# Optimization experiments

Hardware: AMD Instinct MI355X
Metric: run time of the kernel (lower is better)

The kernel has to match this reference:

```python
import jax, jax.numpy as jnp
import numpy as np

# RT-DETR multi-scale deformable attention reference (PPMSDeformableAttention forward, value_mask=None)
SPATIAL_SHAPES = ((80, 80), (40, 40), (20, 20))  # (H, W) per level; sum(H*W) = 8400 = Len_v
NUM_HEADS = 8
NUM_LEVELS = 3
NUM_POINTS = 4


def _gather_corner(v_l, ix, iy, H, W):
    # v_l: [bs, heads, H*W, hd]; ix/iy: [bs, heads, N] int32 pixel indices (possibly out of range)
    valid = (ix >= 0) & (ix < W) & (iy >= 0) & (iy < H)
    idx = jnp.clip(iy, 0, H - 1) * W + jnp.clip(ix, 0, W - 1)
    g = jnp.take_along_axis(v_l, idx[..., None], axis=2)  # [bs, heads, N, hd]
    return jnp.where(valid[..., None], g, jnp.zeros((), v_l.dtype))


def _bilinear_sample(v_l, px, py, H, W):
    # grid_sample(align_corners=False, padding_mode='zeros') semantics.
    # v_l: [bs, heads, H*W, hd]; px/py: [bs, heads, N] continuous pixel coords
    x0 = jnp.floor(px).astype(jnp.int32)
    y0 = jnp.floor(py).astype(jnp.int32)
    x1, y1 = x0 + 1, y0 + 1
    wx1 = px - x0.astype(px.dtype)
    wy1 = py - y0.astype(py.dtype)
    wx0, wy0 = 1.0 - wx1, 1.0 - wy1
    out = (_gather_corner(v_l, x0, y0, H, W) * (wx0 * wy0)[..., None]
           + _gather_corner(v_l, x1, y0, H, W) * (wx1 * wy0)[..., None]
           + _gather_corner(v_l, x0, y1, H, W) * (wx0 * wy1)[..., None]
           + _gather_corner(v_l, x1, y1, H, W) * (wx1 * wy1)[..., None])
    return out  # [bs, heads, N, hd]


def setup_inputs() -> dict:
    key = jax.random.key(0)
    ks = jax.random.split(key, 8)
    bs, Lq, C = 32, 300, 256
    Lv = sum(h * w for h, w in SPATIAL_SHAPES)
    tp = NUM_HEADS * NUM_LEVELS * NUM_POINTS  # 96
    s = 1.0 / np.sqrt(C)
    return {
        "query": jax.random.normal(ks[0], (bs, Lq, C), jnp.float32),
        "reference_points": jax.random.uniform(ks[1], (bs, Lq, NUM_LEVELS, 4), jnp.float32, 0.05, 0.95),
        "value": jax.random.normal(ks[2], (bs, Lv, C), jnp.float32),
        "Wv": jax.random.normal(ks[3], (C, C), jnp.float32) * s,
        "bv": jnp.zeros((C,), jnp.float32),
        "Woff": jax.random.normal(ks[4], (C, tp * 2), jnp.float32) * (s * 0.1),
        "boff": jax.random.normal(ks[5], (tp * 2,), jnp.float32) * 0.5,
        "Watt": jax.random.normal(ks[6], (C, tp), jnp.float32) * s,
        "batt": jnp.zeros((tp,), jnp.float32),
        "Wout": jax.random.normal(ks[7], (C, C), jnp.float32) * s,
        "bout": jnp.zeros((C,), jnp.float32),
    }


def reference(query, reference_points, value, Wv, bv, Woff, boff, Watt, batt, Wout, bout):
    bs, Lq, C = query.shape
    H_, L, P = NUM_HEADS, NUM_LEVELS, NUM_POINTS
    hd = C // H_
    Lv = value.shape[1]

    # value projection -> [bs, heads, Lv, hd]
    v = (value @ Wv + bv).reshape(bs, Lv, H_, hd).transpose(0, 2, 1, 3)

    # sampling offsets and attention weights from query
    off = (query @ Woff + boff).reshape(bs, Lq, H_, L, P, 2)
    attw = jax.nn.softmax((query @ Watt + batt).reshape(bs, Lq, H_, L * P), axis=-1)
    attw = attw.reshape(bs, Lq, H_, L, P)

    # reference_points last dim == 4: (cx, cy, w, h) normalized
    ref_xy = reference_points[:, :, None, :, None, :2]  # [bs,Lq,1,L,1,2]
    ref_wh = reference_points[:, :, None, :, None, 2:]
    loc = ref_xy + off / P * ref_wh * 0.5  # [bs,Lq,H,L,P,2], normalized [0,1]

    out = jnp.zeros((bs, Lq, H_, hd), query.dtype)
    start = 0
    for l, (H, W) in enumerate(SPATIAL_SHAPES):
        v_l = v[:, :, start:start + H * W]  # [bs, heads, H*W, hd]
        start += H * W
        # normalized -> pixel coords (align_corners=False): p = loc * size - 0.5
        locl = loc[:, :, :, l]  # [bs, Lq, heads, P, 2]
        px = locl[..., 0] * W - 0.5
        py = locl[..., 1] * H - 0.5
        # [bs, Lq, heads, P] -> [bs, heads, Lq*P]
        px = px.transpose(0, 2, 1, 3).reshape(bs, H_, Lq * P)
        py = py.transpose(0, 2, 1, 3).reshape(bs, H_, Lq * P)
        sampled = _bilinear_sample(v_l, px, py, H, W)  # [bs, heads, Lq*P, hd]
        sampled = sampled.reshape(bs, H_, Lq, P, hd)
        out = out + jnp.einsum('bhqpd,bqhp->bqhd', sampled, attw[:, :, :, l])

    out = out.reshape(bs, Lq, C)
    return out @ Wout + bout
```

## Files before the change

kernel.cpp:

```cpp
#include <hip/hip_runtime.h>
#include <hip/hip_bf16.h>

#define BS 32
#define LQ 300
#define CDIM 256
#define HEADS 8
#define HD 32
#define NLEVELS 3
#define NPOINTS 4
#define LV 8400
#define NOA 288

typedef __attribute__((ext_vector_type(4))) float f32x4;
typedef __attribute__((ext_vector_type(8))) short short8;
typedef __attribute__((ext_vector_type(8))) unsigned short u16x8;
typedef __attribute__((ext_vector_type(4))) unsigned short u16x4;

__device__ __forceinline__ unsigned short f2bf(float f) {
    __hip_bfloat16 h = __float2bfloat16(f);
    return __bfloat16_as_ushort(h);
}
__device__ __forceinline__ float bf2f(unsigned short u) {
    union { unsigned u; float f; } v; v.u = ((unsigned)u) << 16;
    return v.f;
}

__global__ void prep_weights_kernel(
    const float* __restrict__ Wv, const float* __restrict__ Wout,
    const float* __restrict__ Woff, const float* __restrict__ Watt,
    unsigned short* __restrict__ WvT, unsigned short* __restrict__ WoutT,
    unsigned short* __restrict__ WoaT)
{
    const int bid = blockIdx.x;
    const int k = threadIdx.x;
    if (bid < 256) {
        WvT[bid * 256 + k] = f2bf(Wv[k * 256 + bid]);
    } else if (bid < 512) {
        const int n = bid - 256;
        WoutT[n * 256 + k] = f2bf(Wout[k * 256 + n]);
    } else {
        const int n = bid - 512;
        const float w = (n < 192) ? Woff[k * 192 + n] : Watt[k * 96 + (n - 192)];
        WoaT[n * 256 + k] = f2bf(w);
    }
}

#define BM 128
#define BK 32
#define PAD 40
#define EP2 136
#define NT (CDIM / BK)

__global__ __launch_bounds__(256) void proj_value_mfma(
    const float* __restrict__ value, const unsigned short* __restrict__ WvT,
    const float* __restrict__ bv, unsigned short* __restrict__ vout)
{
    __shared__ alignas(16) unsigned short lds_raw[20480];
    unsigned short* lds_w = lds_raw;
    unsigned short* lds_x = lds_raw + 2 * 128 * PAD;
    unsigned short* lds_ep = lds_raw;

    const int tid = threadIdx.x;
    const int lane = tid & 63;
    const int wave = tid >> 6;
    const int wn = wave & 1;
    const int wm = wave >> 1;
    const int la = lane & 15;
    const int lg = lane >> 4;

    const int orig = blockIdx.x;
    const int xcd = orig & 7, lin = orig >> 3;
    const int bid = xcd * 525 + lin;
    const int n0 = (bid & 1) * 128;
    const long row0 = (long)(bid >> 1) * BM;

    const int sr = tid >> 1;
    const int sk = (tid & 1) * 16;
    const unsigned short* wptr = WvT + (size_t)(n0 + sr) * CDIM + sk;
    const float* xptr = value + (row0 + sr) * (long)CDIM + sk;

    u16x8 wrg[2];
    f32x4 xrg[4];

    auto load_tile = [&](int kb) {
        const u16x8* qw = (const u16x8*)(wptr + kb);
        wrg[0] = qw[0]; wrg[1] = qw[1];
        const float* p = xptr + kb;
        xrg[0] = *(const f32x4*)(p);
        xrg[1] = *(const f32x4*)(p + 4);
        xrg[2] = *(const f32x4*)(p + 8);
        xrg[3] = *(const f32x4*)(p + 12);
    };
    auto write_tile = [&](int buf) {
        u16x8* ww = (u16x8*)&lds_w[buf * (128 * PAD) + sr * PAD + sk];
        ww[0] = wrg[0]; ww[1] = wrg[1];
        u16x8 t0, t1;
#pragma unroll
        for (int i = 0; i < 4; ++i) {
            t0[i]     = f2bf(xrg[0][i]);
            t0[i + 4] = f2bf(xrg[1][i]);
            t1[i]     = f2bf(xrg[2][i]);
            t1[i + 4] = f2bf(xrg[3][i]);
        }
        u16x8* wx = (u16x8*)&lds_x[buf * (128 * PAD) + sr * PAD + sk];
        wx[0] = t0; wx[1] = t1;
    };

    f32x4 acc[4][4] = {};

    load_tile(0);
    write_tile(0);
    __syncthreads();
    int cur = 0;

    for (int t = 0; t < NT; ++t) {
        if (t + 1 < NT) load_tile((t + 1) * BK);

        const unsigned short* pw = &lds_w[cur * (128 * PAD) + (wn * 64 + la) * PAD + lg * 8];
        const unsigned short* px = &lds_x[cur * (128 * PAD) + (wm * 64 + la) * PAD + lg * 8];
        short8 xf[4];
#pragma unroll
        for (int mf = 0; mf < 4; ++mf)
            xf[mf] = *(const short8*)(px + mf * 16 * PAD);
#pragma unroll
        for (int nf = 0; nf < 4; ++nf) {
            const short8 wf = *(const short8*)(pw + nf * 16 * PAD);
#pragma unroll
            for (int mf = 0; mf < 4; ++mf)
                acc[nf][mf] = __builtin_amdgcn_mfma_f32_16x16x32_bf16(wf, xf[mf], acc[nf][mf], 0, 0, 0);
        }

        if (t + 1 < NT) write_tile(cur ^ 1);
        __syncthreads();
        cur ^= 1;
    }

#pragma unroll
    for (int nf = 0; nf < 4; ++nf) {
        const int nbl = wn * 64 + nf * 16 + lg * 4;
        const f32x4 bb = *(const f32x4*)&bv[n0 + nbl];
#pragma unroll
        for (int mf = 0; mf < 4; ++mf) {
            const int mloc = wm * 64 + mf * 16 + la;
            u16x4 o;
#pragma unroll
            for (int j = 0; j < 4; ++j) o[j] = f2bf(acc[nf][mf][j] + bb[j]);
            *(u16x4*)&lds_ep[mloc * EP2 + nbl] = o;
        }
    }
    __syncthreads();
    {
        const int er = tid >> 1;
        const int ec = (tid & 1) * 64;
        const u16x8* src = (const u16x8*)&lds_ep[er * EP2 + ec];
        u16x8* dst = (u16x8*)&vout[(row0 + er) * CDIM + n0 + ec];
#pragma unroll
        for (int i = 0; i < 8; ++i) dst[i] = src[i];
    }
}

#define APAD 40
#define BPAD 40

__global__ __launch_bounds__(256) void offatt_gemm_mfma(
    const float* __restrict__ query, const unsigned short* __restrict__ WoaT,
    const float* __restrict__ boff, const float* __restrict__ batt,
    float* __restrict__ offatt)
{
    __shared__ unsigned short lds_a[2][BM * APAD];
    __shared__ unsigned short lds_b[2][NOA * BPAD];

    const int tid = threadIdx.x;
    const int lane = tid & 63;
    const int wave = tid >> 6;
    const int wm = wave >> 1;
    const int wn = wave & 1;
    const long row0 = (long)blockIdx.x * BM;

    const int ar = tid >> 1;
    const int ak = (tid & 1) * 16;
    const float* aptr = query + (row0 + ar) * CDIM + ak;
    const unsigned short* bptr  = WoaT + (size_t)tid * CDIM;
    const unsigned short* bptr2 = WoaT + (size_t)(256 + tid) * CDIM;
    const bool extra = tid < 32;

    f32x4 arg[4];
    u16x8 brg[4], brg2[4];

    auto load_tile = [&](int kb) {
        const float* p = aptr + kb;
        arg[0] = *(const f32x4*)(p);
        arg[1] = *(const f32x4*)(p + 4);
        arg[2] = *(const f32x4*)(p + 8);
        arg[3] = *(const f32x4*)(p + 12);
        const u16x8* q = (const u16x8*)(bptr + kb);
        brg[0] = q[0]; brg[1] = q[1]; brg[2] = q[2]; brg[3] = q[3];
        if (extra) {
            const u16x8* q2 = (const u16x8*)(bptr2 + kb);
            brg2[0] = q2[0]; brg2[1] = q2[1]; brg2[2] = q2[2]; brg2[3] = q2[3];
        }
    };
    auto write_tile = [&](int buf) {
        u16x8 t0, t1;
#pragma unroll
        for (int i = 0; i < 4; ++i) {
            t0[i]     = f2bf(arg[0][i]);
            t0[i + 4] = f2bf(arg[1][i]);
            t1[i]     = f2bf(arg[2][i]);
            t1[i + 4] = f2bf(arg[3][i]);
        }
        u16x8* wa = (u16x8*)&lds_a[buf][ar * APAD + ak];
        wa[0] = t0; wa[1] = t1;
        u16x8* wb = (u16x8*)&lds_b[buf][tid * BPAD];
        wb[0] = brg[0]; wb[1] = brg[1]; wb[2] = brg[2]; wb[3] = brg[3];
        if (extra) {
            u16x8* wb2 = (u16x8*)&lds_b[buf][(256 + tid) * BPAD];
            wb2[0] = brg2[0]; wb2[1] = brg2[1]; wb2[2] = brg2[2]; wb2[3] = brg2[3];
        }
    };

    f32x4 acc[4][9] = {};
    const int la = lane & 15;
    const int lg = lane >> 4;

    load_tile(0);
    write_tile(0);
    __syncthreads();
    int cur = 0;

    for (int t = 0; t < CDIM / BK; ++t) {
        if (t + 1 < CDIM / BK) load_tile((t + 1) * BK);

        const unsigned short* pa = &lds_a[cur][(wm * 64 + la) * APAD + lg * 8];
        const unsigned short* pb = &lds_b[cur][(wn * 144 + la) * BPAD + lg * 8];
        short8 af[4];
#pragma unroll
        for (int mi = 0; mi < 4; ++mi)
            af[mi] = *(const short8*)(pa + mi * 16 * APAD);
#pragma unroll
        for (int ni = 0; ni < 9; ++ni) {
            const short8 bf = *(const short8*)(pb + ni * 16 * BPAD);
#pragma unroll
            for (int mi = 0; mi < 4; ++mi)
                acc[mi][ni] = __builtin_amdgcn_mfma_f32_16x16x32_bf16(af[mi], bf, acc[mi][ni], 0, 0, 0);
        }

        if (t + 1 < CDIM / BK) write_tile(cur ^ 1);
        __syncthreads();
        cur ^= 1;
    }

    float bias[9];
#pragma unroll
    for (int ni = 0; ni < 9; ++ni) {
        const int col = wn * 144 + ni * 16 + la;
        bias[ni] = (col < 192) ? boff[col] : batt[col - 192];
    }
#pragma unroll
    for (int mi = 0; mi < 4; ++mi) {
#pragma unroll
        for (int ni = 0; ni < 9; ++ni) {
            const int col = wn * 144 + ni * 16 + la;
#pragma unroll
            for (int j = 0; j < 4; ++j) {
                const long r = row0 + wm * 64 + mi * 16 + lg * 4 + j;
                offatt[r * NOA + col] = acc[mi][ni][j] + bias[ni];
            }
        }
    }
}

__global__ __launch_bounds__(256) void sample_kernel(
    const float* __restrict__ offatt, const float* __restrict__ refpts,
    const unsigned short* __restrict__ v, unsigned short* __restrict__ mid)
{
    __shared__ float oa_s[NOA];
    __shared__ float aw_s[96];
    __shared__ float px_s[96];
    __shared__ float py_s[96];

    const int tid = threadIdx.x;
    const int nb = blockIdx.x;
    const int x = nb & 7;
    const int rest = nb >> 3;
    const int g = rest / LQ;
    const int q = rest % LQ;
    const int b = g * 8 + x;
    const long bq = (long)b * LQ + q;

    oa_s[tid] = offatt[bq * NOA + tid];
    if (tid < 32) oa_s[256 + tid] = offatt[bq * NOA + 256 + tid];
    __syncthreads();

    if (tid < 8) {
        float m = -1e30f;
#pragma unroll
        for (int i = 0; i < 12; ++i) m = fmaxf(m, oa_s[192 + tid * 12 + i]);
        float e[12];
        float s = 0.f;
#pragma unroll
        for (int i = 0; i < 12; ++i) { e[i] = __expf(oa_s[192 + tid * 12 + i] - m); s += e[i]; }
        const float inv = 1.f / s;
#pragma unroll
        for (int i = 0; i < 12; ++i) aw_s[tid * 12 + i] = e[i] * inv;
    }
    if (tid >= 128 && tid < 224) {
        const int t = tid - 128;
        const int h = t / 12, idx = t % 12, l = idx >> 2, p = idx & 3;
        const float* rp = refpts + (bq * NLEVELS + l) * 4;
        const float rx = rp[0], ry = rp[1], rw = rp[2], rh = rp[3];
        const float ox = oa_s[((h * NLEVELS + l) * NPOINTS + p) * 2 + 0];
        const float oy = oa_s[((h * NLEVELS + l) * NPOINTS + p) * 2 + 1];
        const float lx = rx + ox * 0.125f * rw;
        const float ly = ry + oy * 0.125f * rh;
        const int Wl = 80 >> l;
        px_s[t] = lx * (float)Wl - 0.5f;
        py_s[t] = ly * (float)Wl - 0.5f;
    }
    __syncthreads();

    const int h = tid >> 5;
    const int pg = (tid >> 3) & 3;
    const int d4 = tid & 7;
    const unsigned short* vb = v + ((size_t)b * LV) * CDIM + h * HD + d4 * 4;

    float a0 = 0.f, a1 = 0.f, a2 = 0.f, a3 = 0.f;
#pragma unroll
    for (int j = 0; j < 3; ++j) {
        const int i = pg * 3 + j;
        const int l = i >> 2;
        const int idx = h * 12 + i;
        const float px = px_s[idx], py = py_s[idx], aw = aw_s[idx];
        const int Wl = 80 >> l;
        const int start = (l == 0) ? 0 : (l == 1) ? 6400 : 8000;

        const float fx = floorf(px), fy = floorf(py);
        const int x0 = (int)fx, y0 = (int)fy;
        const float wx1 = px - fx, wy1 = py - fy;
        const float wx0 = 1.f - wx1, wy0 = 1.f - wy1;
        const float w00 = wx0 * wy0 * aw, w10 = wx1 * wy0 * aw;
        const float w01 = wx0 * wy1 * aw, w11 = wx1 * wy1 * aw;
        const bool x0v = (unsigned)x0 < (unsigned)Wl;
        const bool x1v = (unsigned)(x0 + 1) < (unsigned)Wl;
        const bool y0v = (unsigned)y0 < (unsigned)Wl;
        const bool y1v = (unsigned)(y0 + 1) < (unsigned)Wl;

        const unsigned short* base = vb + (size_t)start * CDIM;
        if (y0v) {
            const unsigned short* r0p = base + (size_t)(y0 * Wl) * CDIM;
            if (x0v) {
                const u16x4 u = *(const u16x4*)(r0p + (size_t)x0 * CDIM);
                a0 = fmaf(w00, bf2f(u[0]), a0); a1 = fmaf(w00, bf2f(u[1]), a1);
                a2 = fmaf(w00, bf2f(u[2]), a2); a3 = fmaf(w00, bf2f(u[3]), a3);
            }
            if (x1v) {
                const u16x4 u = *(const u16x4*)(r0p + (size_t)(x0 + 1) * CDIM);
                a0 = fmaf(w10, bf2f(u[0]), a0); a1 = fmaf(w10, bf2f(u[1]), a1);
                a2 = fmaf(w10, bf2f(u[2]), a2); a3 = fmaf(w10, bf2f(u[3]), a3);
            }
        }
        if (y1v) {
            const unsigned short* r1p = base + (size_t)((y0 + 1) * Wl) * CDIM;
            if (x0v) {
                const u16x4 u = *(const u16x4*)(r1p + (size_t)x0 * CDIM);
                a0 = fmaf(w01, bf2f(u[0]), a0); a1 = fmaf(w01, bf2f(u[1]), a1);
                a2 = fmaf(w01, bf2f(u[2]), a2); a3 = fmaf(w01, bf2f(u[3]), a3);
            }
            if (x1v) {
                const u16x4 u = *(const u16x4*)(r1p + (size_t)(x0 + 1) * CDIM);
                a0 = fmaf(w11, bf2f(u[0]), a0); a1 = fmaf(w11, bf2f(u[1]), a1);
                a2 = fmaf(w11, bf2f(u[2]), a2); a3 = fmaf(w11, bf2f(u[3]), a3);
            }
        }
    }

    a0 += __shfl_xor(a0, 8);  a1 += __shfl_xor(a1, 8);
    a2 += __shfl_xor(a2, 8);  a3 += __shfl_xor(a3, 8);
    a0 += __shfl_xor(a0, 16); a1 += __shfl_xor(a1, 16);
    a2 += __shfl_xor(a2, 16); a3 += __shfl_xor(a3, 16);

    if (pg == 0) {
        u16x4 o;
        o[0] = f2bf(a0); o[1] = f2bf(a1); o[2] = f2bf(a2); o[3] = f2bf(a3);
        *(u16x4*)&mid[bq * CDIM + h * HD + d4 * 4] = o;
    }
}

__global__ __launch_bounds__(256) void out_gemm_mfma(
    const unsigned short* __restrict__ mid, const unsigned short* __restrict__ WoutT,
    const float* __restrict__ bout, float* __restrict__ out)
{
    __shared__ unsigned short lds_w[2][256 * APAD];
    __shared__ unsigned short lds_x[2][BM * BPAD];

    const int tid = threadIdx.x;
    const int lane = tid & 63;
    const int wave = tid >> 6;
    const int wn = wave & 1;
    const int wm = wave >> 1;
    const long row0 = (long)blockIdx.x * BM;

    const unsigned short* wptr = WoutT + (size_t)tid * CDIM;
    const int xr = tid >> 1;
    const int xk = (tid & 1) * 16;
    const unsigned short* xptr = mid + (row0 + xr) * CDIM + xk;

    u16x8 wrg[4];
    u16x8 xrg[2];

    auto load_tile = [&](int kb) {
        const u16x8* qw = (const u16x8*)(wptr + kb);
        wrg[0] = qw[0]; wrg[1] = qw[1]; wrg[2] = qw[2]; wrg[3] = qw[3];
        const u16x8* qx = (const u16x8*)(xptr + kb);
        xrg[0] = qx[0]; xrg[1] = qx[1];
    };
    auto write_tile = [&](int buf) {
        u16x8* ww = (u16x8*)&lds_w[buf][tid * APAD];
        ww[0] = wrg[0]; ww[1] = wrg[1]; ww[2] = wrg[2]; ww[3] = wrg[3];
        u16x8* wx = (u16x8*)&lds_x[buf][xr * BPAD + xk];
        wx[0] = xrg[0]; wx[1] = xrg[1];
    };

    f32x4 acc[8][4] = {};
    const int la = lane & 15;
    const int lg = lane >> 4;

    load_tile(0);
    write_tile(0);
    __syncthreads();
    int cur = 0;

    for (int t = 0; t < CDIM / BK; ++t) {
        if (t + 1 < CDIM / BK) load_tile((t + 1) * BK);

        const unsigned short* pw = &lds_w[cur][(wn * 128 + la) * APAD + lg * 8];
        const unsigned short* px = &lds_x[cur][(wm * 64 + la) * BPAD + lg * 8];
        short8 xf[4];
#pragma unroll
        for (int mf = 0; mf < 4; ++mf)
            xf[mf] = *(const short8*)(px + mf * 16 * BPAD);
#pragma unroll
        for (int nf = 0; nf < 8; ++nf) {
            const short8 wf = *(const short8*)(pw + nf * 16 * APAD);
#pragma unroll
            for (int mf = 0; mf < 4; ++mf)
                acc[nf][mf] = __builtin_amdgcn_mfma_f32_16x16x32_bf16(wf, xf[mf], acc[nf][mf], 0, 0, 0);
        }

        if (t + 1 < CDIM / BK) write_tile(cur ^ 1);
        __syncthreads();
        cur ^= 1;
    }

#pragma unroll
    for (int nf = 0; nf < 8; ++nf) {
        const int nbase = wn * 128 + nf * 16 + lg * 4;
        const f32x4 bb = *(const f32x4*)&bout[nbase];
#pragma unroll
        for (int mf = 0; mf < 4; ++mf) {
            const long m = row0 + wm * 64 + mf * 16 + la;
            f32x4 o;
#pragma unroll
            for (int j = 0; j < 4; ++j) o[j] = acc[nf][mf][j] + bb[j];
            *(f32x4*)&out[m * CDIM + nbase] = o;
        }
    }
}

extern "C" void kernel_launch(void* const* d_in, const int* in_sizes, int n_in,
                              void* d_out, int out_size, void* d_ws, size_t ws_size,
                              hipStream_t stream) {
    const float* query = (const float*)d_in[0];
    const float* refp  = (const float*)d_in[1];
    const float* value = (const float*)d_in[2];
    const float* Wv    = (const float*)d_in[3];
    const float* bv    = (const float*)d_in[4];
    const float* Woff  = (const float*)d_in[5];
    const float* boff  = (const float*)d_in[6];
    const float* Watt  = (const float*)d_in[7];
    const float* batt  = (const float*)d_in[8];
    const float* Wout  = (const float*)d_in[9];
    const float* bout  = (const float*)d_in[10];
    float* out = (float*)d_out;

    char* ws = (char*)d_ws;
    unsigned short* v = (unsigned short*)ws;
    size_t off = (size_t)BS * LV * CDIM * 2;
    float* offatt = (float*)(ws + off);
    off += (size_t)BS * LQ * NOA * 4;
    unsigned short* mid = (unsigned short*)(ws + off);
    off += (size_t)BS * LQ * CDIM * 2;
    unsigned short* WvT = (unsigned short*)(ws + off);
    off += 256 * 256 * 2;
    unsigned short* WoaT = (unsigned short*)(ws + off);
    off += NOA * 256 * 2;
    unsigned short* WoutT = (unsigned short*)(ws + off);

    prep_weights_kernel<<<800, 256, 0, stream>>>(Wv, Wout, Woff, Watt, WvT, WoutT, WoaT);
    proj_value_mfma<<<(BS * LV) / BM * 2, 256, 0, stream>>>(value, WvT, bv, v);
    offatt_gemm_mfma<<<(BS * LQ) / BM, 256, 0, stream>>>(query, WoaT, boff, batt, offatt);
    sample_kernel<<<BS * LQ, 256, 0, stream>>>(offatt, refp, v, mid);
    out_gemm_mfma<<<(BS * LQ) / BM, 256, 0, stream>>>(mid, WoutT, bout, out);
}
```

Baseline: 216.1 us.

## Stream value-projection tiles via global_load_lds into a swizzled triple-buffered LDS pipeline

Rewrites the value-projection GEMM's main loop. Tiles now go straight from global memory into LDS with global_load_lds, triple-buffered two tiles ahead, and synchronised with explicit vmcnt waits and barriers. The fp32 value tile is kept as fp32 in LDS and converted to bf16 when each fragment is read. The weight transpose now writes an XOR-swizzled layout so the unpadded LDS reads avoid bank conflicts. This removes the register staging and the separate LDS write pass, at the cost of 72KB of dynamic LDS (capped at two blocks per CU) and repeated conversion work inside the compute step.

```diff
diff --git a/kernel.cpp b/kernel.cpp
--- a/kernel.cpp
+++ b/kernel.cpp
@@ -24,6 +24,17 @@
     union { unsigned u; float f; } v; v.u = ((unsigned)u) << 16;
     return v.f;
 }
+__device__ __forceinline__ short8 cvt8(const f32x4 a, const f32x4 b) {
+    u16x8 c;
+#pragma unroll
+    for (int i = 0; i < 4; ++i) { c[i] = f2bf(a[i]); c[i + 4] = f2bf(b[i]); }
+    union { u16x8 u; short8 s; } v; v.u = c; return v.s;
+}
+__device__ __forceinline__ void gload16(const void* g, void* l) {
+    __builtin_amdgcn_global_load_lds(
+        (const __attribute__((address_space(1))) void*)g,
+        (__attribute__((address_space(3))) void*)l, 16, 0, 0);
+}
 
 __global__ void prep_weights_kernel(
     const float* __restrict__ Wv, const float* __restrict__ Wout,
@@ -34,7 +45,9 @@
     const int bid = blockIdx.x;
     const int k = threadIdx.x;
     if (bid < 256) {
-        WvT[bid * 256 + k] = f2bf(Wv[k * 256 + bid]);
+        const int n = bid;
+        const int kd = (k & ~31) | ((((k >> 2) & 7) ^ (n & 7)) << 2) | (k & 3);
+        WvT[n * 256 + kd] = f2bf(Wv[k * 256 + n]);
     } else if (bid < 512) {
         const int n = bid - 256;
         WoutT[n * 256 + k] = f2bf(Wout[k * 256 + n]);
@@ -47,18 +60,17 @@
 
 #define BM 128
 #define BK 32
-#define PAD 40
 #define EP2 136
 #define NT (CDIM / BK)
-
-__global__ __launch_bounds__(256) void proj_value_mfma(
+#define TSLOT 24576
+#define WOFF 16384
+#define PROJ_LDS (3 * TSLOT)
+
+__global__ __launch_bounds__(256, 2) void proj_value_mfma(
     const float* __restrict__ value, const unsigned short* __restrict__ WvT,
     const float* __restrict__ bv, unsigned short* __restrict__ vout)
 {
-    __shared__ alignas(16) unsigned short lds_raw[20480];
-    unsigned short* lds_w = lds_raw;
-    unsigned short* lds_x = lds_raw + 2 * 128 * PAD;
-    unsigned short* lds_ep = lds_raw;
+    extern __shared__ char dlds[];
 
     const int tid = threadIdx.x;
     const int lane = tid & 63;
@@ -67,6 +79,7 @@
     const int wm = wave >> 1;
     const int la = lane & 15;
     const int lg = lane >> 4;
+    const int l = lane;
 
     const int orig = blockIdx.x;
     const int xcd = orig & 7, lin = orig >> 3;
@@ -74,82 +87,81 @@
     const int n0 = (bid & 1) * 128;
     const long row0 = (long)(bid >> 1) * BM;
 
-    const int sr = tid >> 1;
-    const int sk = (tid & 1) * 16;
-    const unsigned short* wptr = WvT + (size_t)(n0 + sr) * CDIM + sk;
-    const float* xptr = value + (row0 + sr) * (long)CDIM + sk;
-
-    u16x8 wrg[2];
-    f32x4 xrg[4];
-
-    auto load_tile = [&](int kb) {
-        const u16x8* qw = (const u16x8*)(wptr + kb);
-        wrg[0] = qw[0]; wrg[1] = qw[1];
-        const float* p = xptr + kb;
-        xrg[0] = *(const f32x4*)(p);
-        xrg[1] = *(const f32x4*)(p + 4);
-        xrg[2] = *(const f32x4*)(p + 8);
-        xrg[3] = *(const f32x4*)(p + 12);
+    const float* xsrc = value + (row0 + wave * 32 + (l >> 3)) * (long)CDIM
+                        + ((l & 7) ^ (l >> 3)) * 4;
+    const unsigned short* wsrc = WvT + (size_t)(n0 + wave * 32 + (l >> 2)) * CDIM
+                                 + (l & 3) * 8;
+
+    auto issue = [&](int slot, int t) {
+        char* sb = dlds + slot * TSLOT;
+        const float* xs = xsrc + t * 32;
+        char* xd = sb + wave * 4096;
+#pragma unroll
+        for (int c = 0; c < 4; ++c)
+            gload16(xs + c * 2048, xd + c * 1024);
+        const unsigned short* wsp = wsrc + t * 32;
+        char* wd = sb + WOFF + wave * 2048;
+#pragma unroll
+        for (int c = 0; c < 2; ++c)
+            gload16(wsp + c * 4096, wd + c * 1024);
     };
-    auto write_tile = [&](int buf) {
-        u16x8* ww = (u16x8*)&lds_w[buf * (128 * PAD) + sr * PAD + sk];
-        ww[0] = wrg[0]; ww[1] = wrg[1];
-        u16x8 t0, t1;
-#pragma unroll
-        for (int i = 0; i < 4; ++i) {
-            t0[i]     = f2bf(xrg[0][i]);
-            t0[i + 4] = f2bf(xrg[1][i]);
-            t1[i]     = f2bf(xrg[2][i]);
-            t1[i + 4] = f2bf(xrg[3][i]);
-        }
-        u16x8* wx = (u16x8*)&lds_x[buf * (128 * PAD) + sr * PAD + sk];
-        wx[0] = t0; wx[1] = t1;
+
+    f32x4 acc[4][4] = {};
+
+    auto compute = [&](int slot) {
+        const char* sb = dlds + slot * TSLOT;
+        short8 xf[4];
+#pragma unroll
+        for (int mf = 0; mf < 4; ++mf) {
+            const int row = wm * 64 + mf * 16 + la;
+            const char* xb = sb + row * 128;
+            const f32x4 a = *(const f32x4*)(xb + (((2 * lg)     ^ (la & 7)) * 16));
+            const f32x4 b = *(const f32x4*)(xb + (((2 * lg + 1) ^ (la & 7)) * 16));
+            xf[mf] = cvt8(a, b);
+        }
+#pragma unroll
+        for (int nf = 0; nf < 4; ++nf) {
+            const int row = wn * 64 + nf * 16 + la;
+            const char* wb = sb + WOFF + row * 64;
+            union { unsigned long long q[2]; short8 s; } wu;
+            wu.q[0] = *(const unsigned long long*)(wb + (((2 * lg)     ^ (la & 7)) * 8));
+            wu.q[1] = *(const unsigned long long*)(wb + (((2 * lg + 1) ^ (la & 7)) * 8));
+#pragma unroll
+            for (int mf = 0; mf < 4; ++mf)
+                acc[nf][mf] = __builtin_amdgcn_mfma_f32_16x16x32_bf16(
+                    wu.s, xf[mf], acc[nf][mf], 0, 0, 0);
+        }
     };
 
-    f32x4 acc[4][4] = {};
-
-    load_tile(0);
-    write_tile(0);
-    __syncthreads();
-    int cur = 0;
-
+    issue(0, 0);
+    issue(1, 1);
+
+#pragma unroll
     for (int t = 0; t < NT; ++t) {
-        if (t + 1 < NT) load_tile((t + 1) * BK);
-
-        const unsigned short* pw = &lds_w[cur * (128 * PAD) + (wn * 64 + la) * PAD + lg * 8];
-        const unsigned short* px = &lds_x[cur * (128 * PAD) + (wm * 64 + la) * PAD + lg * 8];
-        short8 xf[4];
-#pragma unroll
-        for (int mf = 0; mf < 4; ++mf)
-            xf[mf] = *(const short8*)(px + mf * 16 * PAD);
-#pragma unroll
-        for (int nf = 0; nf < 4; ++nf) {
-            const short8 wf = *(const short8*)(pw + nf * 16 * PAD);
-#pragma unroll
-            for (int mf = 0; mf < 4; ++mf)
-                acc[nf][mf] = __builtin_amdgcn_mfma_f32_16x16x32_bf16(wf, xf[mf], acc[nf][mf], 0, 0, 0);
-        }
-
-        if (t + 1 < NT) write_tile(cur ^ 1);
-        __syncthreads();
-        cur ^= 1;
-    }
-
-#pragma unroll
-    for (int nf = 0; nf < 4; ++nf) {
-        const int nbl = wn * 64 + nf * 16 + lg * 4;
-        const f32x4 bb = *(const f32x4*)&bv[n0 + nbl];
-#pragma unroll
-        for (int mf = 0; mf < 4; ++mf) {
-            const int mloc = wm * 64 + mf * 16 + la;
-            u16x4 o;
-#pragma unroll
-            for (int j = 0; j < 4; ++j) o[j] = f2bf(acc[nf][mf][j] + bb[j]);
-            *(u16x4*)&lds_ep[mloc * EP2 + nbl] = o;
-        }
-    }
+        if (t < NT - 1) { asm volatile("s_waitcnt vmcnt(6)" ::: "memory"); }
+        else            { asm volatile("s_waitcnt vmcnt(0)" ::: "memory"); }
+        __builtin_amdgcn_s_barrier();
+        if (t + 2 < NT) issue((t + 2) % 3, t + 2);
+        compute(t % 3);
+    }
+
     __syncthreads();
     {
+        unsigned short* lds_ep = (unsigned short*)dlds;
+#pragma unroll
+        for (int nf = 0; nf < 4; ++nf) {
+            const int nbl = wn * 64 + nf * 16 + lg * 4;
+            const f32x4 bb = *(const f32x4*)&bv[n0 + nbl];
+#pragma unroll
+            for (int mf = 0; mf < 4; ++mf) {
+                const int mloc = wm * 64 + mf * 16 + la;
+                u16x4 o;
+#pragma unroll
+                for (int j = 0; j < 4; ++j) o[j] = f2bf(acc[nf][mf][j] + bb[j]);
+                *(u16x4*)&lds_ep[mloc * EP2 + nbl] = o;
+            }
+        }
+        __syncthreads();
         const int er = tid >> 1;
         const int ec = (tid & 1) * 64;
         const u16x8* src = (const u16x8*)&lds_ep[er * EP2 + ec];
@@ -306,14 +318,14 @@
     }
     if (tid >= 128 && tid < 224) {
         const int t = tid - 128;
-        const int h = t / 12, idx = t % 12, l = idx >> 2, p = idx & 3;
-        const float* rp = refpts + (bq * NLEVELS + l) * 4;
+        const int h = t / 12, idx = t % 12, lvl = idx >> 2, p = idx & 3;
+        const float* rp = refpts + (bq * NLEVELS + lvl) * 4;
         const float rx = rp[0], ry = rp[1], rw = rp[2], rh = rp[3];
-        const float ox = oa_s[((h * NLEVELS + l) * NPOINTS + p) * 2 + 0];
-        const float oy = oa_s[((h * NLEVELS + l) * NPOINTS + p) * 2 + 1];
+        const float ox = oa_s[((h * NLEVELS + lvl) * NPOINTS + p) * 2 + 0];
+        const float oy = oa_s[((h * NLEVELS + lvl) * NPOINTS + p) * 2 + 1];
         const float lx = rx + ox * 0.125f * rw;
         const float ly = ry + oy * 0.125f * rh;
-        const int Wl = 80 >> l;
+        const int Wl = 80 >> lvl;
         px_s[t] = lx * (float)Wl - 0.5f;
         py_s[t] = ly * (float)Wl - 0.5f;
     }
@@ -328,11 +340,11 @@
 #pragma unroll
     for (int j = 0; j < 3; ++j) {
         const int i = pg * 3 + j;
-        const int l = i >> 2;
+        const int lvl = i >> 2;
         const int idx = h * 12 + i;
         const float px = px_s[idx], py = py_s[idx], aw = aw_s[idx];
-        const int Wl = 80 >> l;
-        const int start = (l == 0) ? 0 : (l == 1) ? 6400 : 8000;
+        const int Wl = 80 >> lvl;
+        const int start = (lvl == 0) ? 0 : (lvl == 1) ? 6400 : 8000;
 
         const float fx = floorf(px), fy = floorf(py);
         const int x0 = (int)fx, y0 = (int)fy;
@@ -496,8 +508,11 @@
     off += NOA * 256 * 2;
     unsigned short* WoutT = (unsigned short*)(ws + off);
 
+    hipFuncSetAttribute((const void*)proj_value_mfma,
+                        hipFuncAttributeMaxDynamicSharedMemorySize, PROJ_LDS);
+
     prep_weights_kernel<<<800, 256, 0, stream>>>(Wv, Wout, Woff, Watt, WvT, WoutT, WoaT);
-    proj_value_mfma<<<(BS * LV) / BM * 2, 256, 0, stream>>>(value, WvT, bv, v);
+    proj_value_mfma<<<(BS * LV) / BM * 2, 256, PROJ_LDS, stream>>>(value, WvT, bv, v);
     offatt_gemm_mfma<<<(BS * LQ) / BM, 256, 0, stream>>>(query, WoaT, boff, batt, offatt);
     sample_kernel<<<BS * LQ, 256, 0, stream>>>(offatt, refp, v, mid);
     out_gemm_mfma<<<(BS * LQ) / BM, 256, 0, stream>>>(mid, WoutT, bout, out);
```

Result: faster. 202.4 us (-6.4%).

## Load value-projection weights directly from global memory into registers, bypassing LDS

Applied to the files above, without the earlier changes.

The value projection GEMM no longer stages the bf16 weight tile through LDS. Each wave now owns 32 output columns and reads its weight fragments straight from global memory (L2-resident) into registers each k-step. Only the activation tile uses LDS, shared across all 8 M-fragments, and the k-loop is fully unrolled. This cuts LDS traffic and footprint but adds per-wave global loads of the weight with less reuse per fragment. Some loop variables in the sampling kernel are renamed.

```diff
diff --git a/kernel.cpp b/kernel.cpp
--- a/kernel.cpp
+++ b/kernel.cpp
@@ -55,16 +55,13 @@
     const float* __restrict__ value, const unsigned short* __restrict__ WvT,
     const float* __restrict__ bv, unsigned short* __restrict__ vout)
 {
-    __shared__ alignas(16) unsigned short lds_raw[20480];
-    unsigned short* lds_w = lds_raw;
-    unsigned short* lds_x = lds_raw + 2 * 128 * PAD;
+    __shared__ alignas(16) unsigned short lds_raw[17408];
+    unsigned short* lds_x = lds_raw;
     unsigned short* lds_ep = lds_raw;
 
     const int tid = threadIdx.x;
     const int lane = tid & 63;
     const int wave = tid >> 6;
-    const int wn = wave & 1;
-    const int wm = wave >> 1;
     const int la = lane & 15;
     const int lg = lane >> 4;
 
@@ -76,15 +73,13 @@
 
     const int sr = tid >> 1;
     const int sk = (tid & 1) * 16;
-    const unsigned short* wptr = WvT + (size_t)(n0 + sr) * CDIM + sk;
     const float* xptr = value + (row0 + sr) * (long)CDIM + sk;
 
-    u16x8 wrg[2];
+    const unsigned short* wlane = WvT + (size_t)(n0 + wave * 32 + la) * CDIM + lg * 8;
+
     f32x4 xrg[4];
 
     auto load_tile = [&](int kb) {
-        const u16x8* qw = (const u16x8*)(wptr + kb);
-        wrg[0] = qw[0]; wrg[1] = qw[1];
         const float* p = xptr + kb;
         xrg[0] = *(const f32x4*)(p);
         xrg[1] = *(const f32x4*)(p + 4);
@@ -92,8 +87,6 @@
         xrg[3] = *(const f32x4*)(p + 12);
     };
     auto write_tile = [&](int buf) {
-        u16x8* ww = (u16x8*)&lds_w[buf * (128 * PAD) + sr * PAD + sk];
-        ww[0] = wrg[0]; ww[1] = wrg[1];
         u16x8 t0, t1;
 #pragma unroll
         for (int i = 0; i < 4; ++i) {
@@ -106,28 +99,30 @@
         wx[0] = t0; wx[1] = t1;
     };
 
-    f32x4 acc[4][4] = {};
+    f32x4 acc[2][8] = {};
 
     load_tile(0);
     write_tile(0);
     __syncthreads();
     int cur = 0;
 
+#pragma unroll
     for (int t = 0; t < NT; ++t) {
         if (t + 1 < NT) load_tile((t + 1) * BK);
 
-        const unsigned short* pw = &lds_w[cur * (128 * PAD) + (wn * 64 + la) * PAD + lg * 8];
-        const unsigned short* px = &lds_x[cur * (128 * PAD) + (wm * 64 + la) * PAD + lg * 8];
-        short8 xf[4];
-#pragma unroll
-        for (int mf = 0; mf < 4; ++mf)
-            xf[mf] = *(const short8*)(px + mf * 16 * PAD);
-#pragma unroll
-        for (int nf = 0; nf < 4; ++nf) {
-            const short8 wf = *(const short8*)(pw + nf * 16 * PAD);
-#pragma unroll
-            for (int mf = 0; mf < 4; ++mf)
-                acc[nf][mf] = __builtin_amdgcn_mfma_f32_16x16x32_bf16(wf, xf[mf], acc[nf][mf], 0, 0, 0);
+        short8 wf[2];
+#pragma unroll
+        for (int nf = 0; nf < 2; ++nf)
+            wf[nf] = *(const short8*)(wlane + (size_t)nf * 16 * CDIM + t * 32);
+
+        const unsigned short* px = &lds_x[cur * (128 * PAD) + la * PAD + lg * 8];
+#pragma unroll
+        for (int mf = 0; mf < 8; ++mf) {
+            const short8 xf = *(const short8*)(px + mf * 16 * PAD);
+#pragma unroll
+            for (int nf = 0; nf < 2; ++nf)
+                acc[nf][mf] = __builtin_amdgcn_mfma_f32_16x16x32_bf16(
+                    wf[nf], xf, acc[nf][mf], 0, 0, 0);
         }
 
         if (t + 1 < NT) write_tile(cur ^ 1);
@@ -136,12 +131,12 @@
     }
 
 #pragma unroll
-    for (int nf = 0; nf < 4; ++nf) {
-        const int nbl = wn * 64 + nf * 16 + lg * 4;
+    for (int nf = 0; nf < 2; ++nf) {
+        const int nbl = wave * 32 + nf * 16 + lg * 4;
         const f32x4 bb = *(const f32x4*)&bv[n0 + nbl];
 #pragma unroll
-        for (int mf = 0; mf < 4; ++mf) {
-            const int mloc = wm * 64 + mf * 16 + la;
+        for (int mf = 0; mf < 8; ++mf) {
+            const int mloc = mf * 16 + la;
             u16x4 o;
 #pragma unroll
             for (int j = 0; j < 4; ++j) o[j] = f2bf(acc[nf][mf][j] + bb[j]);
@@ -306,14 +301,14 @@
     }
     if (tid >= 128 && tid < 224) {
         const int t = tid - 128;
-        const int h = t / 12, idx = t % 12, l = idx >> 2, p = idx & 3;
-        const float* rp = refpts + (bq * NLEVELS + l) * 4;
+        const int h = t / 12, idx = t % 12, lvl = idx >> 2, p = idx & 3;
+        const float* rp = refpts + (bq * NLEVELS + lvl) * 4;
         const float rx = rp[0], ry = rp[1], rw = rp[2], rh = rp[3];
-        const float ox = oa_s[((h * NLEVELS + l) * NPOINTS + p) * 2 + 0];
-        const float oy = oa_s[((h * NLEVELS + l) * NPOINTS + p) * 2 + 1];
+        const float ox = oa_s[((h * NLEVELS + lvl) * NPOINTS + p) * 2 + 0];
+        const float oy = oa_s[((h * NLEVELS + lvl) * NPOINTS + p) * 2 + 1];
         const float lx = rx + ox * 0.125f * rw;
         const float ly = ry + oy * 0.125f * rh;
-        const int Wl = 80 >> l;
+        const int Wl = 80 >> lvl;
         px_s[t] = lx * (float)Wl - 0.5f;
         py_s[t] = ly * (float)Wl - 0.5f;
     }
@@ -328,11 +323,11 @@
 #pragma unroll
     for (int j = 0; j < 3; ++j) {
         const int i = pg * 3 + j;
-        const int l = i >> 2;
+        const int lvl = i >> 2;
         const int idx = h * 12 + i;
         const float px = px_s[idx], py = py_s[idx], aw = aw_s[idx];
-        const int Wl = 80 >> l;
-        const int start = (l == 0) ? 0 : (l == 1) ? 6400 : 8000;
+        const int Wl = 80 >> lvl;
+        const int start = (lvl == 0) ? 0 : (lvl == 1) ? 6400 : 8000;
 
         const float fx = floorf(px), fy = floorf(py);
         const int x0 = (int)fx, y0 = (int)fy;
```

Result: no change. 216.7 us (+0.3%).
